# Kernel optimization log

Measured on AMD Instinct MI355X. Metric: run time of the kernel, lower is better.

The kernel has to match this reference:

```python
import jax, jax.numpy as jnp
import numpy as np

D_MODEL = 1024
N_HEAD = 16
D_K = 64
D_V = 64
SEQ = 4096


def setup_inputs() -> dict:
    key = jax.random.key(0)
    ks = jax.random.split(key, 7)
    s = 1.0 / np.sqrt(D_MODEL)
    return {
        "q": jax.random.normal(ks[0], (SEQ, D_MODEL), dtype=jnp.float32),
        "k": jax.random.normal(ks[1], (SEQ, D_MODEL), dtype=jnp.float32),
        "v": jax.random.normal(ks[2], (SEQ, D_MODEL), dtype=jnp.float32),
        "Wq": jax.random.normal(ks[3], (N_HEAD * D_K, D_MODEL), dtype=jnp.float32) * s,
        "Wk": jax.random.normal(ks[4], (N_HEAD * D_K, D_MODEL), dtype=jnp.float32) * s,
        "Wv": jax.random.normal(ks[5], (N_HEAD * D_V, D_MODEL), dtype=jnp.float32) * s,
        "Wfc": jax.random.normal(ks[6], (D_MODEL, N_HEAD * D_V), dtype=jnp.float32) * s,
    }


def reference(q, k, v, Wq, Wk, Wv, Wfc):
    len_q = q.shape[0]
    residual = q
    temperature = jnp.asarray(np.sqrt(D_K), q.dtype)
    # projections: [len, n_head, d_k] -> [n_head, len, d_k]
    qh = (q @ Wq.T).reshape(len_q, N_HEAD, D_K).transpose(1, 0, 2)
    kh = (k @ Wk.T).reshape(k.shape[0], N_HEAD, D_K).transpose(1, 0, 2)
    vh = (v @ Wv.T).reshape(v.shape[0], N_HEAD, D_V).transpose(1, 0, 2)
    # scores: [n_head, len_q, len_k]
    attn = jnp.einsum('hqd,hkd->hqk', qh / temperature, kh)
    attn = jax.nn.softmax(attn, axis=-1)  # dropout = identity (eval)
    out = jnp.einsum('hqk,hkd->hqd', attn, vh)  # [n_head, len_q, d_v]
    out = out.transpose(1, 0, 2).reshape(len_q, N_HEAD * D_V)
    out = out @ Wfc.T  # dropout = identity (eval)
    return jax.nn.relu(out) + residual
```

## Files before the change

### kernel.cpp

```cpp
#include <hip/hip_runtime.h>
#include <math.h>

#define SEQ    4096
#define DMODEL 1024
#define NHEAD  16
#define DHEAD  64
#define KVHALF 2048

typedef __bf16 bf16;
typedef bf16  bf16x2 __attribute__((ext_vector_type(2)));
typedef bf16  bf16x4 __attribute__((ext_vector_type(4)));
typedef bf16  bf16x8 __attribute__((ext_vector_type(8)));
typedef float f32x4  __attribute__((ext_vector_type(4)));
typedef float f32x16 __attribute__((ext_vector_type(16)));
typedef unsigned int u32;

#define SWZ(r)  ((((r) >> 2) ^ (r)) & 7)
#define SWZ3(r) (((r) ^ ((r) >> 2) ^ ((r) >> 3)) & 7)

__device__ __forceinline__ void gll16(const void* g, void* l) {
    __builtin_amdgcn_global_load_lds(
        (const __attribute__((address_space(1))) void*)g,
        (__attribute__((address_space(3))) void*)l, 16, 0, 0);
}

__device__ __forceinline__ u32 cvtpk(float lo, float hi) {
    u32 r;
    asm("v_cvt_pk_bf16_f32 %0, %1, %2" : "=v"(r) : "v"(lo), "v"(hi));
    return r;
}
__device__ __forceinline__ void pswap(u32& a, u32& b) {
    asm volatile("v_permlane32_swap_b32 %0, %1" : "+v"(a), "+v"(b));
}

__global__ __launch_bounds__(256)
void cvt_all(const float* __restrict__ q, const float* __restrict__ k,
             const float* __restrict__ v, const float* __restrict__ Wq,
             const float* __restrict__ Wk, const float* __restrict__ Wv,
             const float* __restrict__ Wfc,
             bf16* __restrict__ qb, bf16* __restrict__ kb, bf16* __restrict__ vb,
             bf16* __restrict__ Wqb, bf16* __restrict__ Wkb, bf16* __restrict__ Wvb,
             bf16* __restrict__ Wfcb)
{
    const int b = blockIdx.x;
    const float* s; bf16* d; int base;
    if      (b < 2048) { s = q;   d = qb;   base = b; }
    else if (b < 4096) { s = k;   d = kb;   base = b - 2048; }
    else if (b < 6144) { s = v;   d = vb;   base = b - 4096; }
    else if (b < 6656) { s = Wq;  d = Wqb;  base = b - 6144; }
    else if (b < 7168) { s = Wk;  d = Wkb;  base = b - 6656; }
    else if (b < 7680) { s = Wv;  d = Wvb;  base = b - 7168; }
    else               { s = Wfc; d = Wfcb; base = b - 7680; }
    const int i = (base * 256 + threadIdx.x) * 8;
    float4 a0 = *(const float4*)&s[i];
    float4 a1 = *(const float4*)&s[i + 4];
    bf16x8 o;
    o[0] = (bf16)a0.x; o[1] = (bf16)a0.y; o[2] = (bf16)a0.z; o[3] = (bf16)a0.w;
    o[4] = (bf16)a1.x; o[5] = (bf16)a1.y; o[6] = (bf16)a1.z; o[7] = (bf16)a1.w;
    *(bf16x8*)&d[i] = o;
}

template<int EPI>
__device__ __forceinline__ void gemm_body(
    const bf16* __restrict__ A, const bf16* __restrict__ B,
    bf16* __restrict__ Cb, float* __restrict__ Cf, const float* __restrict__ res)
{
    constexpr int N = DMODEL, K = DMODEL;
    const int bm   = blockIdx.y * 64;
    const int bn   = blockIdx.x * 64;
    const int tid  = threadIdx.x;
    const int w    = tid >> 6;
    const int lane = tid & 63;
    const int lr   = lane & 15;
    const int lh   = lane >> 4;
    const int wr   = w >> 1;
    const int wc   = w & 1;
    const int lrow = lane >> 3;
    const int lch  = lane & 7;

    __shared__ bf16 As[64 * 64];
    __shared__ bf16 Bs[64 * 64];

    f32x4 acc[2][2] = {};

    for (int k0 = 0; k0 < K; k0 += 64) {
        __syncthreads();
        #pragma unroll
        for (int i = 0; i < 2; ++i) {
            const int r = (w * 2 + i) * 8 + lrow;
            gll16(A + (size_t)(bm + r) * K + k0 + ((lch ^ SWZ(r)) << 3),
                  &As[(w * 2 + i) * 512]);
        }
        #pragma unroll
        for (int i = 0; i < 2; ++i) {
            const int r = (w * 2 + i) * 8 + lrow;
            gll16(B + (size_t)(bn + r) * K + k0 + ((lch ^ SWZ(r)) << 3),
                  &Bs[(w * 2 + i) * 512]);
        }
        asm volatile("s_waitcnt vmcnt(0)" ::: "memory");
        __syncthreads();

        bf16x8 af[2][2], bfr[2][2];
        #pragma unroll
        for (int rt = 0; rt < 2; ++rt)
            #pragma unroll
            for (int s = 0; s < 2; ++s) {
                const int r = wr * 32 + rt * 16 + lr;
                af[rt][s] = *(const bf16x8*)&As[r * 64 + (((s * 4 + lh) ^ SWZ(r)) << 3)];
            }
        #pragma unroll
        for (int ct = 0; ct < 2; ++ct)
            #pragma unroll
            for (int s = 0; s < 2; ++s) {
                const int r = wc * 32 + ct * 16 + lr;
                bfr[ct][s] = *(const bf16x8*)&Bs[r * 64 + (((s * 4 + lh) ^ SWZ(r)) << 3)];
            }
        __builtin_amdgcn_s_setprio(1);
        #pragma unroll
        for (int rt = 0; rt < 2; ++rt)
            #pragma unroll
            for (int ct = 0; ct < 2; ++ct)
                #pragma unroll
                for (int s = 0; s < 2; ++s)
                    acc[rt][ct] = __builtin_amdgcn_mfma_f32_16x16x32_bf16(
                        af[rt][s], bfr[ct][s], acc[rt][ct], 0, 0, 0);
        __builtin_amdgcn_s_setprio(0);
    }

    #pragma unroll
    for (int rt = 0; rt < 2; ++rt)
        #pragma unroll
        for (int ct = 0; ct < 2; ++ct)
            #pragma unroll
            for (int r = 0; r < 4; ++r) {
                const int m = bm + wr * 32 + rt * 16 + lh * 4 + r;
                const int n = bn + wc * 32 + ct * 16 + lr;
                if (EPI == 0) {
                    Cb[(size_t)m * N + n] = (bf16)acc[rt][ct][r];
                } else {
                    Cf[(size_t)m * N + n] =
                        fmaxf(acc[rt][ct][r], 0.f) + res[(size_t)m * N + n];
                }
            }
}

__global__ __launch_bounds__(256)
void gemm_qkv(const bf16* __restrict__ qb, const bf16* __restrict__ kb,
              const bf16* __restrict__ vb, const bf16* __restrict__ Wqb,
              const bf16* __restrict__ Wkb, const bf16* __restrict__ Wvb,
              bf16* __restrict__ Pq, bf16* __restrict__ Pk, bf16* __restrict__ Pv)
{
    const bf16 *A, *B; bf16* C;
    if      (blockIdx.z == 0) { A = qb; B = Wqb; C = Pq; }
    else if (blockIdx.z == 1) { A = kb; B = Wkb; C = Pk; }
    else                      { A = vb; B = Wvb; C = Pv; }
    gemm_body<0>(A, B, C, nullptr, nullptr);
}

__global__ __launch_bounds__(256)
void gemm_fc(const bf16* __restrict__ AO, const bf16* __restrict__ Wfcb,
             float* __restrict__ out, const float* __restrict__ res)
{
    gemm_body<1>(AO, Wfcb, nullptr, out, res);
}

__global__ __launch_bounds__(256, 4)
void attn_mfma(const bf16* __restrict__ Q, const bf16* __restrict__ K,
               const bf16* __restrict__ V,
               bf16* __restrict__ Oa, bf16* __restrict__ Ob,
               float* __restrict__ La, float* __restrict__ Lb)
{
    const int wg   = blockIdx.x;
    const int lgc  = (wg & 7) * 128 + (wg >> 3);
    const int half = lgc >> 9;
    const int h    = (lgc >> 5) & 15;
    const int q0   = (lgc & 31) * 128;
    const int c0   = half * KVHALF;

    bf16*  Op = half ? Ob : Oa;
    float* Lp = half ? Lb : La;

    const int tid  = threadIdx.x;
    const int w    = tid >> 6;
    const int lane = tid & 63;
    const int lo5  = lane & 31;
    const int hi   = lane >> 5;
    const int lrow = lane >> 3;
    const int lch  = lane & 7;

    __shared__ bf16 Ks[2][64 * 64];
    __shared__ bf16 Vt[2][64 * 64];

    const bf16* qrow = Q + (size_t)(q0 + w * 32 + lo5) * DMODEL + h * 64;
    bf16x8 qf[4];
    #pragma unroll
    for (int s = 0; s < 4; ++s)
        qf[s] = *(const bf16x8*)&qrow[s * 16 + hi * 8];

    f32x16 acc0 = {}, acc1 = {};
    float lsum = 0.f;

    const int vk = (tid & 7) * 8;
    const int vd = (tid >> 3) * 2;

    const float SC = 0.18033688f;

    #pragma unroll
    for (int i = 0; i < 2; ++i) {
        const int r = (w * 2 + i) * 8 + lrow;
        gll16(K + (size_t)(c0 + r) * DMODEL + h * 64 + ((lch ^ SWZ3(r)) << 3),
              &Ks[0][(w * 2 + i) * 512]);
    }
    {
        bf16x2 u[8];
        #pragma unroll
        for (int i = 0; i < 8; ++i)
            u[i] = *(const bf16x2*)&V[(size_t)(c0 + vk + i) * DMODEL + h * 64 + vd];
        asm volatile("s_waitcnt vmcnt(0)" ::: "memory");
        bf16x8 v0, v1;
        #pragma unroll
        for (int i = 0; i < 8; ++i) { v0[i] = u[i][0]; v1[i] = u[i][1]; }
        *(bf16x8*)&Vt[0][(vd + 0) * 64 + (((tid & 7) ^ SWZ3(vd + 0)) << 3)] = v0;
        *(bf16x8*)&Vt[0][(vd + 1) * 64 + (((tid & 7) ^ SWZ3(vd + 1)) << 3)] = v1;
    }
    __syncthreads();

#define BODY(CUR, CN)                                                          \
    {                                                                          \
        const int cn = c0 + (((CN) - c0) & (KVHALF - 1));                      \
        _Pragma("unroll")                                                      \
        for (int i = 0; i < 2; ++i) {                                          \
            const int r = (w * 2 + i) * 8 + lrow;                              \
            gll16(K + (size_t)(cn + r) * DMODEL + h * 64 + ((lch ^ SWZ3(r)) << 3), \
                  &Ks[(CUR) ^ 1][(w * 2 + i) * 512]);                          \
        }                                                                      \
        bf16x2 u[8];                                                           \
        _Pragma("unroll")                                                      \
        for (int i = 0; i < 8; ++i)                                            \
            u[i] = *(const bf16x2*)&V[(size_t)(cn + vk + i) * DMODEL + h * 64 + vd]; \
        const bf16* Kc = Ks[CUR];                                              \
        const bf16* Vc = Vt[CUR];                                              \
        _Pragma("unroll")                                                      \
        for (int kh = 0; kh < 2; ++kh) {                                       \
            const int rr = kh * 32 + lo5;                                      \
            f32x16 st = {};                                                    \
            __builtin_amdgcn_s_setprio(1);                                     \
            _Pragma("unroll")                                                  \
            for (int s = 0; s < 4; ++s) {                                      \
                bf16x8 kf = *(const bf16x8*)&Kc[rr * 64 + (((s * 2 + hi) ^ SWZ3(rr)) << 3)]; \
                st = __builtin_amdgcn_mfma_f32_32x32x16_bf16(kf, qf[s], st, 0, 0, 0); \
            }                                                                  \
            __builtin_amdgcn_s_setprio(0);                                     \
            _Pragma("unroll")                                                  \
            for (int r = 0; r < 16; ++r)                                       \
                st[r] = __builtin_amdgcn_exp2f(fminf(st[r] * SC, 50.f));       \
            lsum += (((st[0] + st[1]) + (st[2] + st[3]))                       \
                   + ((st[4] + st[5]) + (st[6] + st[7])))                      \
                  + (((st[8] + st[9]) + (st[10] + st[11]))                     \
                   + ((st[12] + st[13]) + (st[14] + st[15])));                 \
            _Pragma("unroll")                                                  \
            for (int kk = 0; kk < 2; ++kk) {                                   \
                const int ks = kh * 2 + kk;                                    \
                const int b = kk * 8;                                          \
                u32 A0 = cvtpk(st[b + 0], st[b + 1]);                          \
                u32 C0 = cvtpk(st[b + 2], st[b + 3]);                          \
                u32 B0 = cvtpk(st[b + 4], st[b + 5]);                          \
                u32 D0 = cvtpk(st[b + 6], st[b + 7]);                          \
                pswap(A0, B0);                                                 \
                pswap(C0, D0);                                                 \
                union { u32 wd[4]; bf16x8 v; } fr;                             \
                fr.wd[0] = A0; fr.wd[1] = C0; fr.wd[2] = B0; fr.wd[3] = D0;    \
                bf16x8 vf0 = *(const bf16x8*)&Vc[lo5 * 64 + (((ks * 2 + hi) ^ SWZ3(lo5)) << 3)]; \
                bf16x8 vf1 = *(const bf16x8*)&Vc[(32 + lo5) * 64 + (((ks * 2 + hi) ^ SWZ3(32 + lo5)) << 3)]; \
                __builtin_amdgcn_s_setprio(1);                                 \
                acc0 = __builtin_amdgcn_mfma_f32_32x32x16_bf16(vf0, fr.v, acc0, 0, 0, 0); \
                acc1 = __builtin_amdgcn_mfma_f32_32x32x16_bf16(vf1, fr.v, acc1, 0, 0, 0); \
                __builtin_amdgcn_s_setprio(0);                                 \
            }                                                                  \
        }                                                                      \
        asm volatile("s_waitcnt vmcnt(0)" ::: "memory");                       \
        {                                                                      \
            bf16x8 v0, v1;                                                     \
            _Pragma("unroll")                                                  \
            for (int i = 0; i < 8; ++i) { v0[i] = u[i][0]; v1[i] = u[i][1]; }  \
            bf16* Vn = Vt[(CUR) ^ 1];                                          \
            *(bf16x8*)&Vn[(vd + 0) * 64 + (((tid & 7) ^ SWZ3(vd + 0)) << 3)] = v0; \
            *(bf16x8*)&Vn[(vd + 1) * 64 + (((tid & 7) ^ SWZ3(vd + 1)) << 3)] = v1; \
        }                                                                      \
        __syncthreads();                                                       \
    }

    for (int c = c0; c < c0 + KVHALF; c += 128) {
        BODY(0, c + 64)
        BODY(1, c + 128)
    }
#undef BODY

    float lt = lsum;
    lt += __shfl_xor(lt, 32);
    Lp[h * SEQ + q0 + w * 32 + lo5] = lt;

    bf16* orow = Op + (size_t)(q0 + w * 32 + lo5) * DMODEL + h * 64;
    #pragma unroll
    for (int g = 0; g < 4; ++g) {
        bf16x4 o4;
        o4[0] = (bf16)acc0[g * 4 + 0];
        o4[1] = (bf16)acc0[g * 4 + 1];
        o4[2] = (bf16)acc0[g * 4 + 2];
        o4[3] = (bf16)acc0[g * 4 + 3];
        *(bf16x4*)&orow[g * 8 + 4 * hi] = o4;
        bf16x4 o5;
        o5[0] = (bf16)acc1[g * 4 + 0];
        o5[1] = (bf16)acc1[g * 4 + 1];
        o5[2] = (bf16)acc1[g * 4 + 2];
        o5[3] = (bf16)acc1[g * 4 + 3];
        *(bf16x4*)&orow[32 + g * 8 + 4 * hi] = o5;
    }
}

__global__ __launch_bounds__(256)
void combine(const bf16* __restrict__ Oa, const bf16* __restrict__ Ob,
             const float* __restrict__ La, const float* __restrict__ Lb,
             bf16* __restrict__ AO)
{
    const int e   = (blockIdx.x * 256 + threadIdx.x) * 8;
    const int row = e >> 10;
    const int hh  = (e >> 6) & 15;
    const float inv = 1.0f / (La[hh * SEQ + row] + Lb[hh * SEQ + row]);
    bf16x8 a = *(const bf16x8*)&Oa[e];
    bf16x8 b = *(const bf16x8*)&Ob[e];
    bf16x8 o;
    #pragma unroll
    for (int i = 0; i < 8; ++i)
        o[i] = (bf16)(((float)a[i] + (float)b[i]) * inv);
    *(bf16x8*)&AO[e] = o;
}

extern "C" void kernel_launch(void* const* d_in, const int* in_sizes, int n_in,
                              void* d_out, int out_size, void* d_ws, size_t ws_size,
                              hipStream_t stream)
{
    const float* q   = (const float*)d_in[0];
    const float* k   = (const float*)d_in[1];
    const float* v   = (const float*)d_in[2];
    const float* Wq  = (const float*)d_in[3];
    const float* Wk  = (const float*)d_in[4];
    const float* Wv  = (const float*)d_in[5];
    const float* Wfc = (const float*)d_in[6];
    float* out = (float*)d_out;

    const int EM = SEQ * DMODEL;
    const int WM = DMODEL * DMODEL;

    bf16* Wfcb = (bf16*)d_ws;
    bf16* qb   = Wfcb + WM;
    bf16* kb   = qb + EM;
    bf16* vb   = kb + EM;
    bf16* Wqb  = vb + EM;
    bf16* Wkb  = Wqb + WM;
    bf16* Wvb  = Wkb + WM;
    bf16* Pq   = Wvb + WM;
    bf16* Pk   = Pq + EM;
    bf16* Pv   = Pk + EM;
    bf16* AO   = Pv + EM;

    bf16*  Oa = qb;
    bf16*  Ob = kb;
    float* La = (float*)vb;
    float* Lb = La + NHEAD * SEQ;

    cvt_all<<<8192, 256, 0, stream>>>(q, k, v, Wq, Wk, Wv, Wfc,
                                      qb, kb, vb, Wqb, Wkb, Wvb, Wfcb);

    gemm_qkv<<<dim3(DMODEL / 64, SEQ / 64, 3), 256, 0, stream>>>(
        qb, kb, vb, Wqb, Wkb, Wvb, Pq, Pk, Pv);

    attn_mfma<<<1024, 256, 0, stream>>>(Pq, Pk, Pv, Oa, Ob, La, Lb);

    combine<<<EM / 2048, 256, 0, stream>>>(Oa, Ob, La, Lb, AO);

    gemm_fc<<<dim3(DMODEL / 64, SEQ / 64), 256, 0, stream>>>(AO, Wfcb, out, q);
}
```

Baseline: 198.0 us.

## Emit V projection pre-transposed in tiles and fold softmax scale into Q

The V projection GEMM now computes Wv·vᵀ and writes V transposed in contiguous 64x64 tiles per head and sequence block. The attention kernel can then load each V tile with two 16-byte vector loads per thread instead of eight strided 4-byte loads plus an in-register transpose. The softmax scale (log2e/sqrt(dk)) is applied in the Q projection epilogue, which removes a multiply per score element in the inner loop. This costs a more scattered tiled-store epilogue in the GEMM, and rounding the pre-scaled Q to bf16 slightly changes numerics.

Result: faster. 179.7 us (-9.2%).

```diff
diff --git a/kernel.cpp b/kernel.cpp
--- a/kernel.cpp
+++ b/kernel.cpp
@@ -8,7 +8,6 @@
 #define KVHALF 2048
 
 typedef __bf16 bf16;
-typedef bf16  bf16x2 __attribute__((ext_vector_type(2)));
 typedef bf16  bf16x4 __attribute__((ext_vector_type(4)));
 typedef bf16  bf16x8 __attribute__((ext_vector_type(8)));
 typedef float f32x4  __attribute__((ext_vector_type(4)));
@@ -17,6 +16,8 @@
 
 #define SWZ(r)  ((((r) >> 2) ^ (r)) & 7)
 #define SWZ3(r) (((r) ^ ((r) >> 2) ^ ((r) >> 3)) & 7)
+
+#define SCQ 0.18033688f
 
 __device__ __forceinline__ void gll16(const void* g, void* l) {
     __builtin_amdgcn_global_load_lds(
@@ -63,11 +64,10 @@
 template<int EPI>
 __device__ __forceinline__ void gemm_body(
     const bf16* __restrict__ A, const bf16* __restrict__ B,
-    bf16* __restrict__ Cb, float* __restrict__ Cf, const float* __restrict__ res)
-{
-    constexpr int N = DMODEL, K = DMODEL;
-    const int bm   = blockIdx.y * 64;
-    const int bn   = blockIdx.x * 64;
+    bf16* __restrict__ Cb, float* __restrict__ Cf, const float* __restrict__ res,
+    int bm, int bn, int N, float scale)
+{
+    constexpr int K = DMODEL;
     const int tid  = threadIdx.x;
     const int w    = tid >> 6;
     const int lane = tid & 63;
@@ -135,11 +135,15 @@
             for (int r = 0; r < 4; ++r) {
                 const int m = bm + wr * 32 + rt * 16 + lh * 4 + r;
                 const int n = bn + wc * 32 + ct * 16 + lr;
+                const float vv = acc[rt][ct][r] * scale;
                 if (EPI == 0) {
-                    Cb[(size_t)m * N + n] = (bf16)acc[rt][ct][r];
+                    Cb[(size_t)m * N + n] = (bf16)vv;
+                } else if (EPI == 2) {
+                    Cb[(((size_t)(m >> 6) * (size_t)(N >> 6) + (size_t)(n >> 6)) << 12)
+                       + ((m & 63) << 6) + (n & 63)] = (bf16)vv;
                 } else {
                     Cf[(size_t)m * N + n] =
-                        fmaxf(acc[rt][ct][r], 0.f) + res[(size_t)m * N + n];
+                        fmaxf(vv, 0.f) + res[(size_t)m * N + n];
                 }
             }
 }
@@ -148,25 +152,30 @@
 void gemm_qkv(const bf16* __restrict__ qb, const bf16* __restrict__ kb,
               const bf16* __restrict__ vb, const bf16* __restrict__ Wqb,
               const bf16* __restrict__ Wkb, const bf16* __restrict__ Wvb,
-              bf16* __restrict__ Pq, bf16* __restrict__ Pk, bf16* __restrict__ Pv)
-{
-    const bf16 *A, *B; bf16* C;
-    if      (blockIdx.z == 0) { A = qb; B = Wqb; C = Pq; }
-    else if (blockIdx.z == 1) { A = kb; B = Wkb; C = Pk; }
-    else                      { A = vb; B = Wvb; C = Pv; }
-    gemm_body<0>(A, B, C, nullptr, nullptr);
+              bf16* __restrict__ Pq, bf16* __restrict__ Pk, bf16* __restrict__ Pvt)
+{
+    if (blockIdx.z == 0)
+        gemm_body<0>(qb, Wqb, Pq, nullptr, nullptr,
+                     blockIdx.y * 64, blockIdx.x * 64, DMODEL, SCQ);
+    else if (blockIdx.z == 1)
+        gemm_body<0>(kb, Wkb, Pk, nullptr, nullptr,
+                     blockIdx.y * 64, blockIdx.x * 64, DMODEL, 1.0f);
+    else
+        gemm_body<2>(Wvb, vb, Pvt, nullptr, nullptr,
+                     blockIdx.x * 64, blockIdx.y * 64, SEQ, 1.0f);
 }
 
 __global__ __launch_bounds__(256)
 void gemm_fc(const bf16* __restrict__ AO, const bf16* __restrict__ Wfcb,
              float* __restrict__ out, const float* __restrict__ res)
 {
-    gemm_body<1>(AO, Wfcb, nullptr, out, res);
+    gemm_body<1>(AO, Wfcb, nullptr, out, res,
+                 blockIdx.y * 64, blockIdx.x * 64, DMODEL, 1.0f);
 }
 
 __global__ __launch_bounds__(256, 4)
 void attn_mfma(const bf16* __restrict__ Q, const bf16* __restrict__ K,
-               const bf16* __restrict__ V,
+               const bf16* __restrict__ Vt_g,
                bf16* __restrict__ Oa, bf16* __restrict__ Ob,
                float* __restrict__ La, float* __restrict__ Lb)
 {
@@ -200,10 +209,12 @@
     f32x16 acc0 = {}, acc1 = {};
     float lsum = 0.f;
 
-    const int vk = (tid & 7) * 8;
-    const int vd = (tid >> 3) * 2;
-
-    const float SC = 0.18033688f;
+    const int vd  = tid >> 2;
+    const int vc2 = (tid & 3) * 2;
+    const int voff = vd * 64 + vc2 * 8;
+    const int vw0 = vd * 64 + (((vc2 + 0) ^ SWZ3(vd)) << 3);
+    const int vw1 = vd * 64 + (((vc2 + 1) ^ SWZ3(vd)) << 3);
+    const bf16* Vth = Vt_g + ((size_t)h * (SEQ / 64) << 12);
 
     #pragma unroll
     for (int i = 0; i < 2; ++i) {
@@ -212,16 +223,12 @@
               &Ks[0][(w * 2 + i) * 512]);
     }
     {
-        bf16x2 u[8];
-        #pragma unroll
-        for (int i = 0; i < 8; ++i)
-            u[i] = *(const bf16x2*)&V[(size_t)(c0 + vk + i) * DMODEL + h * 64 + vd];
+        const bf16* vt = Vth + (((size_t)(c0 >> 6)) << 12);
+        bf16x8 u0 = *(const bf16x8*)&vt[voff];
+        bf16x8 u1 = *(const bf16x8*)&vt[voff + 8];
         asm volatile("s_waitcnt vmcnt(0)" ::: "memory");
-        bf16x8 v0, v1;
-        #pragma unroll
-        for (int i = 0; i < 8; ++i) { v0[i] = u[i][0]; v1[i] = u[i][1]; }
-        *(bf16x8*)&Vt[0][(vd + 0) * 64 + (((tid & 7) ^ SWZ3(vd + 0)) << 3)] = v0;
-        *(bf16x8*)&Vt[0][(vd + 1) * 64 + (((tid & 7) ^ SWZ3(vd + 1)) << 3)] = v1;
+        *(bf16x8*)&Vt[0][vw0] = u0;
+        *(bf16x8*)&Vt[0][vw1] = u1;
     }
     __syncthreads();
 
@@ -234,10 +241,9 @@
             gll16(K + (size_t)(cn + r) * DMODEL + h * 64 + ((lch ^ SWZ3(r)) << 3), \
                   &Ks[(CUR) ^ 1][(w * 2 + i) * 512]);                          \
         }                                                                      \
-        bf16x2 u[8];                                                           \
-        _Pragma("unroll")                                                      \
-        for (int i = 0; i < 8; ++i)                                            \
-            u[i] = *(const bf16x2*)&V[(size_t)(cn + vk + i) * DMODEL + h * 64 + vd]; \
+        const bf16* vt = Vth + (((size_t)(cn >> 6)) << 12);                    \
+        bf16x8 u0 = *(const bf16x8*)&vt[voff];                                 \
+        bf16x8 u1 = *(const bf16x8*)&vt[voff + 8];                             \
         const bf16* Kc = Ks[CUR];                                              \
         const bf16* Vc = Vt[CUR];                                              \
         _Pragma("unroll")                                                      \
@@ -253,7 +259,7 @@
             __builtin_amdgcn_s_setprio(0);                                     \
             _Pragma("unroll")                                                  \
             for (int r = 0; r < 16; ++r)                                       \
-                st[r] = __builtin_amdgcn_exp2f(fminf(st[r] * SC, 50.f));       \
+                st[r] = __builtin_amdgcn_exp2f(fminf(st[r], 50.f));            \
             lsum += (((st[0] + st[1]) + (st[2] + st[3]))                       \
                    + ((st[4] + st[5]) + (st[6] + st[7])))                      \
                   + (((st[8] + st[9]) + (st[10] + st[11]))                     \
@@ -280,12 +286,9 @@
         }                                                                      \
         asm volatile("s_waitcnt vmcnt(0)" ::: "memory");                       \
         {                                                                      \
-            bf16x8 v0, v1;                                                     \
-            _Pragma("unroll")                                                  \
-            for (int i = 0; i < 8; ++i) { v0[i] = u[i][0]; v1[i] = u[i][1]; }  \
             bf16* Vn = Vt[(CUR) ^ 1];                                          \
-            *(bf16x8*)&Vn[(vd + 0) * 64 + (((tid & 7) ^ SWZ3(vd + 0)) << 3)] = v0; \
-            *(bf16x8*)&Vn[(vd + 1) * 64 + (((tid & 7) ^ SWZ3(vd + 1)) << 3)] = v1; \
+            *(bf16x8*)&Vn[vw0] = u0;                                           \
+            *(bf16x8*)&Vn[vw1] = u1;                                           \
         }                                                                      \
         __syncthreads();                                                       \
     }
@@ -361,8 +364,8 @@
     bf16* Wvb  = Wkb + WM;
     bf16* Pq   = Wvb + WM;
     bf16* Pk   = Pq + EM;
-    bf16* Pv   = Pk + EM;
-    bf16* AO   = Pv + EM;
+    bf16* Pvt  = Pk + EM;
+    bf16* AO   = Pvt + EM;
 
     bf16*  Oa = qb;
     bf16*  Ob = kb;
@@ -373,9 +376,9 @@
                                       qb, kb, vb, Wqb, Wkb, Wvb, Wfcb);
 
     gemm_qkv<<<dim3(DMODEL / 64, SEQ / 64, 3), 256, 0, stream>>>(
-        qb, kb, vb, Wqb, Wkb, Wvb, Pq, Pk, Pv);
-
-    attn_mfma<<<1024, 256, 0, stream>>>(Pq, Pk, Pv, Oa, Ob, La, Lb);
+        qb, kb, vb, Wqb, Wkb, Wvb, Pq, Pk, Pvt);
+
+    attn_mfma<<<1024, 256, 0, stream>>>(Pq, Pk, Pvt, Oa, Ob, La, Lb);
 
     combine<<<EM / 2048, 256, 0, stream>>>(Oa, Ob, La, Lb, AO);
 
```
